# Performance work log

Measured on AMD Instinct MI355X. Metric: run time of the kernel, lower is better.

## Reference

```python
import jax, jax.numpy as jnp
import numpy as np

EPS = 1e-6
NEG_SLOPE = 0.2


def knn_idx(xf, k):
    # xf: (B, C, N) flattened vector features; returns (B, N, k) neighbor indices
    xx = jnp.sum(xf * xf, axis=1)                       # (B, N)
    inner = jnp.einsum('bcn,bcm->bnm', xf, xf)          # (B, N, N)
    neg_dist = 2.0 * inner - xx[:, :, None] - xx[:, None, :]  # -||xi-xj||^2
    _, idx = jax.lax.top_k(neg_dist, k)                 # includes self (dist 0)
    return idx


def get_graph_feature(x, k):
    # x: (B, D, 3, N) -> edge features (B, 2D, 3, N, k)
    B, D, _, N = x.shape
    idx = knn_idx(x.reshape(B, D * 3, N), k)            # (B, N, k)
    pts = jnp.transpose(x, (0, 3, 1, 2))                # (B, N, D, 3)
    neigh = jax.vmap(lambda p, i: p[i])(pts, idx)       # (B, N, k, D, 3) gather
    center = jnp.broadcast_to(pts[:, :, None], neigh.shape)
    feat = jnp.concatenate([neigh - center, center], axis=3)  # (B, N, k, 2D, 3)
    return jnp.transpose(feat, (0, 3, 4, 1, 2))


def vn_linear_leakyrelu(x, Wf, Wd):
    # Vector-Neuron linear + leaky ReLU. x: (B, Cin, 3, ...),
    # Wf: (Cout, Cin), Wd: (Cout, Cin) or (1, Cin) when nonlinearity is shared.
    p = jnp.einsum('oi,bi...->bo...', Wf, x)
    d = jnp.einsum('oi,bi...->bo...', Wd, x)
    dot = jnp.sum(p * d, axis=2, keepdims=True)
    dsq = jnp.sum(d * d, axis=2, keepdims=True)
    proj = p - (dot / (dsq + EPS)) * d
    return NEG_SLOPE * p + (1.0 - NEG_SLOPE) * jnp.where(dot >= 0, p, proj)


def setup_inputs() -> dict:
    key = jax.random.key(0)
    ks = jax.random.split(key, 11)
    B, N = 8, 1024
    x = jax.random.normal(ks[0], (B, 3, N), dtype=jnp.float32)
    # dims = [1, 21, 21, 42, 85, 341]
    ins = [2, 42, 42, 84, 169]      # 2*dim_in for edge layers; sum(dims[1:-1]) for last
    outs = [21, 21, 42, 85, 341]
    dirs = [21, 21, 42, 85, 1]      # last layer has share_nonlinearity=True
    d = {"x": x}
    for i, (ci, co, cd) in enumerate(zip(ins, outs, dirs)):
        s = 1.0 / np.sqrt(ci)
        kf, kd = jax.random.split(ks[1 + i])
        d[f"Wf{i}"] = (jax.random.normal(kf, (co, ci), dtype=jnp.float32) * s)
        d[f"Wd{i}"] = (jax.random.normal(kd, (cd, ci), dtype=jnp.float32) * s)
    d["k"] = 20
    return d


def reference(x, Wf0, Wd0, Wf1, Wd1, Wf2, Wd2, Wf3, Wd3, Wf4, Wd4, k):
    cur = x[:, None]                 # (B, 1, 3, N)
    feats = []
    for Wf, Wd in ((Wf0, Wd0), (Wf1, Wd1), (Wf2, Wd2), (Wf3, Wd3)):
        g = get_graph_feature(cur, k)        # (B, 2D, 3, N, k)
        h = vn_linear_leakyrelu(g, Wf, Wd)   # (B, Dout, 3, N, k)
        cur = h.mean(axis=-1)                # mean over neighbors -> (B, Dout, 3, N)
        feats.append(cur)
    xcat = jnp.concatenate(feats, axis=1)    # (B, 169, 3, N)
    out = vn_linear_leakyrelu(xcat, Wf4, Wd4)
    return out.mean(axis=-1)                 # mean over points -> (B, 341, 3)
```

## Files before the change

kernel.cpp:

```cpp
#include <hip/hip_runtime.h>
#include <cstddef>

#define BB 8
#define NN 1024
#define KK 20
#define CCAT 169
#define NT 16

__global__ __launch_bounds__(256) void dist_tile_kernel(
    const float* __restrict__ src, int bs, int F, float* __restrict__ dist) {
  __shared__ float As[8][128];
  __shared__ float Bs[8][128];
  int b = blockIdx.z;
  int rem = blockIdx.x, bi = 0;
  while (rem >= 8 - bi) { rem -= 8 - bi; ++bi; }
  int bj = bi + rem;
  int n0 = bi * 128;
  int m0 = bj * 128;
  int t = threadIdx.x;
  int tx = t & 15, ty = t >> 4;
  const float* p = src + (size_t)b * bs;

  float acc[8][8];
  float xn[8], xm[8];
#pragma unroll
  for (int i = 0; i < 8; ++i) {
    xn[i] = 0.f;
    xm[i] = 0.f;
#pragma unroll
    for (int j = 0; j < 8; ++j) acc[i][j] = 0.f;
  }

  int fr = t >> 5;
  int cc = (t & 31) << 2;
  for (int f0 = 0; f0 < F; f0 += 8) {
    int f = f0 + fr;
    float4 av = {0.f, 0.f, 0.f, 0.f}, bv = {0.f, 0.f, 0.f, 0.f};
    if (f < F) {
      av = *(const float4*)(p + (size_t)f * NN + n0 + cc);
      bv = *(const float4*)(p + (size_t)f * NN + m0 + cc);
    }
    __syncthreads();
    *(float4*)&As[fr][cc] = av;
    *(float4*)&Bs[fr][cc] = bv;
    __syncthreads();
#pragma unroll
    for (int f2 = 0; f2 < 8; ++f2) {
      float4 al = *(const float4*)&As[f2][ty << 2];
      float4 ah = *(const float4*)&As[f2][64 + (ty << 2)];
      float4 bl = *(const float4*)&Bs[f2][tx << 2];
      float4 bh = *(const float4*)&Bs[f2][64 + (tx << 2)];
      float a[8] = {al.x, al.y, al.z, al.w, ah.x, ah.y, ah.z, ah.w};
      float bb[8] = {bl.x, bl.y, bl.z, bl.w, bh.x, bh.y, bh.z, bh.w};
#pragma unroll
      for (int i = 0; i < 8; ++i) xn[i] += a[i] * a[i];
#pragma unroll
      for (int j = 0; j < 8; ++j) xm[j] += bb[j] * bb[j];
#pragma unroll
      for (int i = 0; i < 8; ++i)
#pragma unroll
        for (int j = 0; j < 8; ++j) acc[i][j] += a[i] * bb[j];
    }
  }

#pragma unroll
  for (int i = 0; i < 8; ++i)
#pragma unroll
    for (int j = 0; j < 8; ++j) acc[i][j] = 2.f * acc[i][j] - xn[i] - xm[j];

#pragma unroll
  for (int i = 0; i < 8; ++i) {
    int n = n0 + ((i < 4) ? ((ty << 2) + i) : (64 + (ty << 2) + i - 4));
    float* dr = dist + (((size_t)b * NN + n) << 10);
    *(float4*)(dr + m0 + (tx << 2)) =
        make_float4(acc[i][0], acc[i][1], acc[i][2], acc[i][3]);
    *(float4*)(dr + m0 + 64 + (tx << 2)) =
        make_float4(acc[i][4], acc[i][5], acc[i][6], acc[i][7]);
  }

  if (bi != bj) {
#pragma unroll
    for (int j = 0; j < 8; ++j) {
      int m = m0 + ((j < 4) ? ((tx << 2) + j) : (64 + (tx << 2) + j - 4));
      float* dr = dist + (((size_t)b * NN + m) << 10);
      *(float4*)(dr + n0 + (ty << 2)) =
          make_float4(acc[0][j], acc[1][j], acc[2][j], acc[3][j]);
      *(float4*)(dr + n0 + 64 + (ty << 2)) =
          make_float4(acc[4][j], acc[5][j], acc[6][j], acc[7][j]);
    }
  }
}

__device__ __forceinline__ unsigned long long shfl_xor_u64(
    unsigned long long v, int off) {
  unsigned lo = (unsigned)v, hi = (unsigned)(v >> 32);
  lo = __shfl_xor(lo, off, 64);
  hi = __shfl_xor(hi, off, 64);
  return ((unsigned long long)hi << 32) | lo;
}

__global__ __launch_bounds__(256) void topk_kernel(
    const float* __restrict__ dist, int* __restrict__ idx_out) {
  int wave = threadIdx.x >> 6;
  int lane = threadIdx.x & 63;
  int row = blockIdx.x * 4 + wave;
  const float* d = dist + ((size_t)row << 10);

  unsigned long long key[16];
#pragma unroll
  for (int s = 0; s < 16; ++s) {
    int m = lane + (s << 6);
    unsigned u = __float_as_uint(d[m]);
    u = (u & 0x80000000u) ? ~u : (u | 0x80000000u);
    key[s] = ((unsigned long long)u << 32) | (unsigned)(NN - 1 - m);
  }

#pragma unroll
  for (int size = 2; size <= 16; size <<= 1) {
#pragma unroll
    for (int stride = size >> 1; stride > 0; stride >>= 1) {
#pragma unroll
      for (int i = 0; i < 16; ++i) {
        int j = i ^ stride;
        if (j > i) {
          unsigned long long a = key[i], c = key[j];
          bool desc = ((i & size) == 0);
          bool sw = desc ? (a < c) : (a > c);
          key[i] = sw ? c : a;
          key[j] = sw ? a : c;
        }
      }
    }
  }

  int* out = idx_out + row * KK;
  unsigned long long head = key[0];
  for (int r = 0; r < KK; ++r) {
    unsigned long long w = head;
#pragma unroll
    for (int off = 32; off > 0; off >>= 1) {
      unsigned long long o = shfl_xor_u64(w, off);
      if (o > w) w = o;
    }
    if (lane == 0) out[r] = (NN - 1) - (int)(w & 0xFFFFFFFFull);
    if (head == w) {
#pragma unroll
      for (int s = 0; s < 15; ++s) key[s] = key[s + 1];
      key[15] = 0ull;
      head = key[0];
    }
  }
}

__global__ __launch_bounds__(256) void edge_fused_kernel(
    const float* __restrict__ src, int bs, int D, int Co, int nsplit,
    const float* __restrict__ Wf, const float* __restrict__ Wd,
    const int* __restrict__ idx, int ooff, float* __restrict__ xcat) {
  __shared__ float2 Ulds[3 * NN];
  __shared__ float2 Vlds[3 * NN];
  __shared__ float4 Wlds[48];
  int bo = blockIdx.x;
  int b = bo / Co, o = bo % Co;
  int t = threadIdx.x;

  if (t < D) {
    float wfa = Wf[o * 2 * D + t];
    float wfb = Wf[o * 2 * D + D + t] - wfa;
    float wda = Wd[o * 2 * D + t];
    float wdb = Wd[o * 2 * D + D + t] - wda;
    Wlds[t] = make_float4(wfa, wfb, wda, wdb);
  }
  __syncthreads();

  const float* sb = src + (size_t)b * bs;
#pragma unroll
  for (int r = 0; r < 3; ++r) {
    int g = t + 256 * r;
    float4 uf = {0.f, 0.f, 0.f, 0.f}, vf = {0.f, 0.f, 0.f, 0.f};
    float4 ud = {0.f, 0.f, 0.f, 0.f}, vd = {0.f, 0.f, 0.f, 0.f};
    for (int i = 0; i < D; ++i) {
      float4 s = *(const float4*)(sb + (size_t)i * 3 * NN + (g << 2));
      float4 w = Wlds[i];
      uf.x += w.x * s.x; uf.y += w.x * s.y; uf.z += w.x * s.z; uf.w += w.x * s.w;
      vf.x += w.y * s.x; vf.y += w.y * s.y; vf.z += w.y * s.z; vf.w += w.y * s.w;
      ud.x += w.z * s.x; ud.y += w.z * s.y; ud.z += w.z * s.z; ud.w += w.z * s.w;
      vd.x += w.w * s.x; vd.y += w.w * s.y; vd.z += w.w * s.z; vd.w += w.w * s.w;
    }
    *(float4*)&Ulds[(g << 2) + 0] = make_float4(uf.x, ud.x, uf.y, ud.y);
    *(float4*)&Ulds[(g << 2) + 2] = make_float4(uf.z, ud.z, uf.w, ud.w);
    *(float4*)&Vlds[(g << 2) + 0] = make_float4(vf.x, vd.x, vf.y, vd.y);
    *(float4*)&Vlds[(g << 2) + 2] = make_float4(vf.z, vd.z, vf.w, vd.w);
  }
  __syncthreads();

  const float inv_k = 1.f / KK;
  int cnt = NN / nsplit;
  int nbase = blockIdx.y * cnt;
  for (int n = nbase + t; n < nbase + cnt; n += 256) {
    float2 v0 = Vlds[n];
    float2 v1 = Vlds[NN + n];
    float2 v2 = Vlds[2 * NN + n];
    const int4* ip = (const int4*)(idx + (b * NN + n) * KK);
    float a0 = 0.f, a1 = 0.f, a2 = 0.f;
#pragma unroll
    for (int q = 0; q < 5; ++q) {
      int4 iv = ip[q];
      int nbs[4] = {iv.x, iv.y, iv.z, iv.w};
#pragma unroll
      for (int jj = 0; jj < 4; ++jj) {
        int nb = nbs[jj];
        float2 u0 = Ulds[nb];
        float2 u1 = Ulds[NN + nb];
        float2 u2 = Ulds[2 * NN + nb];
        float pf0 = u0.x + v0.x, pd0 = u0.y + v0.y;
        float pf1 = u1.x + v1.x, pd1 = u1.y + v1.y;
        float pf2 = u2.x + v2.x, pd2 = u2.y + v2.y;
        float dot = pf0 * pd0 + pf1 * pd1 + pf2 * pd2;
        float dsq = pd0 * pd0 + pd1 * pd1 + pd2 * pd2;
        float g = (dot >= 0.f) ? 0.f : 0.8f * dot / (dsq + 1e-6f);
        a0 += pf0 - g * pd0;
        a1 += pf1 - g * pd1;
        a2 += pf2 - g * pd2;
      }
    }
    size_t ob = (size_t)b * CCAT * 3 * NN + (size_t)(ooff + o) * 3 * NN + n;
    xcat[ob] = a0 * inv_k;
    xcat[ob + NN] = a1 * inv_k;
    xcat[ob + 2 * NN] = a2 * inv_k;
  }
}

__global__ __launch_bounds__(256) void final_fused_kernel(
    const float* __restrict__ xcat, const float* __restrict__ Wf4,
    const float* __restrict__ Wd4, float* __restrict__ part) {
  __shared__ float Ws[16][64];
  __shared__ float Xs[3][16][64];
  __shared__ float Wds[16];
  int b = blockIdx.z;
  int o0 = blockIdx.y * 64;
  int n0 = blockIdx.x * 64;
  int t = threadIdx.x;
  int tx = t & 15, ty = t >> 4;

  float acc[3][4][4];
  float dv[3][4];
#pragma unroll
  for (int c = 0; c < 3; ++c) {
#pragma unroll
    for (int i = 0; i < 4; ++i)
#pragma unroll
      for (int j = 0; j < 4; ++j) acc[c][i][j] = 0.f;
#pragma unroll
    for (int j = 0; j < 4; ++j) dv[c][j] = 0.f;
  }

  const float* xb = xcat + (size_t)b * CCAT * 3 * NN;
  for (int f0 = 0; f0 < CCAT; f0 += 16) {
    int f = f0 + ty;
    float4 xv[3];
#pragma unroll
    for (int c = 0; c < 3; ++c) {
      xv[c] = make_float4(0.f, 0.f, 0.f, 0.f);
      if (f < CCAT)
        xv[c] = *(const float4*)(xb + ((size_t)f * 3 + c) * NN + n0 + (tx << 2));
    }
    float wv[4];
#pragma unroll
    for (int q = 0; q < 4; ++q) {
      int o = o0 + (tx << 2) + q;
      wv[q] = (o < 341 && f < CCAT) ? Wf4[o * CCAT + f] : 0.f;
    }
    float wdv = 0.f;
    if (t < 16 && f0 + t < CCAT) wdv = Wd4[f0 + t];
    __syncthreads();
#pragma unroll
    for (int c = 0; c < 3; ++c) *(float4*)&Xs[c][ty][tx << 2] = xv[c];
    *(float4*)&Ws[ty][tx << 2] = make_float4(wv[0], wv[1], wv[2], wv[3]);
    if (t < 16) Wds[t] = wdv;
    __syncthreads();
#pragma unroll
    for (int f2 = 0; f2 < 16; ++f2) {
      float4 w = *(const float4*)&Ws[f2][ty << 2];
      float wa[4] = {w.x, w.y, w.z, w.w};
      float wd = Wds[f2];
#pragma unroll
      for (int c = 0; c < 3; ++c) {
        float4 x = *(const float4*)&Xs[c][f2][tx << 2];
        float xa[4] = {x.x, x.y, x.z, x.w};
#pragma unroll
        for (int j = 0; j < 4; ++j) dv[c][j] += wd * xa[j];
#pragma unroll
        for (int i = 0; i < 4; ++i)
#pragma unroll
          for (int j = 0; j < 4; ++j) acc[c][i][j] += wa[i] * xa[j];
      }
    }
  }

  float s[3][4];
#pragma unroll
  for (int c = 0; c < 3; ++c)
#pragma unroll
    for (int i = 0; i < 4; ++i) s[c][i] = 0.f;
#pragma unroll
  for (int i = 0; i < 4; ++i) {
#pragma unroll
    for (int j = 0; j < 4; ++j) {
      float d0 = dv[0][j], d1 = dv[1][j], d2 = dv[2][j];
      float p0 = acc[0][i][j], p1 = acc[1][i][j], p2 = acc[2][i][j];
      float dot = p0 * d0 + p1 * d1 + p2 * d2;
      float dsq = d0 * d0 + d1 * d1 + d2 * d2;
      float g = (dot >= 0.f) ? 0.f : 0.8f * dot / (dsq + 1e-6f);
      s[0][i] += p0 - g * d0;
      s[1][i] += p1 - g * d1;
      s[2][i] += p2 - g * d2;
    }
  }

#pragma unroll
  for (int off = 1; off < 16; off <<= 1) {
#pragma unroll
    for (int c = 0; c < 3; ++c)
#pragma unroll
      for (int i = 0; i < 4; ++i) s[c][i] += __shfl_xor(s[c][i], off, 64);
  }
  if (tx == 0) {
#pragma unroll
    for (int i = 0; i < 4; ++i) {
      int o = o0 + (ty << 2) + i;
      if (o < 341) {
#pragma unroll
        for (int c = 0; c < 3; ++c)
          part[(((size_t)b * 341 + o) * 3 + c) * NT + blockIdx.x] = s[c][i];
      }
    }
  }
}

__global__ void final_reduce_kernel(const float* __restrict__ part,
                                    float* __restrict__ out) {
  int t = blockIdx.x * 256 + threadIdx.x;
  if (t >= BB * 341 * 3) return;
  const float* p = part + (size_t)t * NT;
  float s = 0.f;
#pragma unroll
  for (int nt = 0; nt < NT; ++nt) s += p[nt];
  out[t] = s * (1.f / 1024.f);
}

extern "C" void kernel_launch(void* const* d_in, const int* in_sizes, int n_in,
                              void* d_out, int out_size, void* d_ws,
                              size_t ws_size, hipStream_t stream) {
  (void)in_sizes; (void)n_in; (void)out_size; (void)ws_size;
  const float* x = (const float*)d_in[0];
  const float* Wf[5] = {(const float*)d_in[1], (const float*)d_in[3],
                        (const float*)d_in[5], (const float*)d_in[7],
                        (const float*)d_in[9]};
  const float* Wd[5] = {(const float*)d_in[2], (const float*)d_in[4],
                        (const float*)d_in[6], (const float*)d_in[8],
                        (const float*)d_in[10]};

  float* ws = (float*)d_ws;
  float* dist = ws;
  float* part = ws;
  size_t off = (size_t)BB * NN * NN;
  int* idx = (int*)(ws + off);
  off += (size_t)BB * NN * KK;
  float* xcat = ws + off;

  struct LayerCfg { int D, Co, inoff, ooff, nsplit; };
  const LayerCfg L[4] = {
      {1, 21, 0, 0, 4},
      {21, 21, 0, 21, 4},
      {21, 42, 21, 42, 2},
      {42, 85, 42, 84, 1},
  };

  for (int l = 0; l < 4; ++l) {
    const float* src = (l == 0) ? x : (xcat + (size_t)L[l].inoff * 3 * NN);
    int bs = (l == 0) ? 3 * NN : CCAT * 3 * NN;
    int D = L[l].D, Co = L[l].Co;

    dist_tile_kernel<<<dim3(36, 1, BB), 256, 0, stream>>>(src, bs, 3 * D, dist);
    topk_kernel<<<(BB * NN) / 4, 256, 0, stream>>>(dist, idx);
    edge_fused_kernel<<<dim3(BB * Co, L[l].nsplit), 256, 0, stream>>>(
        src, bs, D, Co, L[l].nsplit, Wf[l], Wd[l], idx, L[l].ooff, xcat);
  }

  final_fused_kernel<<<dim3(NT, 6, BB), 256, 0, stream>>>(xcat, Wf[4], Wd[4],
                                                          part);
  final_reduce_kernel<<<(BB * 341 * 3 + 255) / 256, 256, 0, stream>>>(
      part, (float*)d_out);
}
```

Before: 431.8 us.

## Split edge kernel into tiled transform GEMM and gather, retile final kernel

The per-output-channel edge kernel, which recomputed the U/V linear transform over the whole point set with a naive per-thread loop, is split into a shared-memory tiled transform kernel that writes U/V to workspace and a gather kernel that loads them into LDS and does the neighbor aggregation. This reuses source feature tiles across 16 output channels instead of re-reading the inputs once per channel. It costs an extra launch and a global round trip for U/V, which reuse the distance-matrix workspace. Separately, the final kernel's output tile is halved to 32 channels to launch more blocks, and the last layer's gather now uses two splits.

```diff
diff --git a/kernel.cpp b/kernel.cpp
--- a/kernel.cpp
+++ b/kernel.cpp
@@ -152,46 +152,98 @@
   }
 }
 
-__global__ __launch_bounds__(256) void edge_fused_kernel(
-    const float* __restrict__ src, int bs, int D, int Co, int nsplit,
+__global__ __launch_bounds__(256) void transform_kernel(
+    const float* __restrict__ src, int bs, int D, int Co,
     const float* __restrict__ Wf, const float* __restrict__ Wd,
-    const int* __restrict__ idx, int ooff, float* __restrict__ xcat) {
-  __shared__ float2 Ulds[3 * NN];
-  __shared__ float2 Vlds[3 * NN];
-  __shared__ float4 Wlds[48];
+    float2* __restrict__ ubuf, float2* __restrict__ vbuf) {
+  __shared__ float4 Slds4[16][32];
+  __shared__ float4 Wlds[16][16];
+  int b = blockIdx.z;
+  int g0 = blockIdx.x * 128;
+  int o0 = blockIdx.y * 16;
+  int t = threadIdx.x;
+  int tx = t & 15, ty = t >> 4;
+  const float* sb = src + (size_t)b * bs;
+
+  float uf[8], ud[8], vf[8], vd[8];
+#pragma unroll
+  for (int g = 0; g < 8; ++g) { uf[g] = 0.f; ud[g] = 0.f; vf[g] = 0.f; vd[g] = 0.f; }
+
+  for (int f0 = 0; f0 < D; f0 += 16) {
+    float4 w4 = {0.f, 0.f, 0.f, 0.f};
+    {
+      int i = f0 + tx;
+      int o = o0 + ty;
+      if (i < D && o < Co) {
+        float wfa = Wf[o * 2 * D + i];
+        float wfb = Wf[o * 2 * D + D + i];
+        float wda = Wd[o * 2 * D + i];
+        float wdb = Wd[o * 2 * D + D + i];
+        w4 = make_float4(wfa, wfb - wfa, wda, wdb - wda);
+      }
+    }
+    int q0 = t, q1 = t + 256;
+    int r0 = q0 >> 5, c0 = q0 & 31;
+    int r1 = q1 >> 5, c1 = q1 & 31;
+    float4 s0 = {0.f, 0.f, 0.f, 0.f}, s1 = {0.f, 0.f, 0.f, 0.f};
+    if (f0 + r0 < D)
+      s0 = *(const float4*)(sb + (size_t)(f0 + r0) * 3 * NN + g0 + (c0 << 2));
+    if (f0 + r1 < D)
+      s1 = *(const float4*)(sb + (size_t)(f0 + r1) * 3 * NN + g0 + (c1 << 2));
+    __syncthreads();
+    Wlds[tx][ty] = w4;
+    Slds4[r0][c0] = s0;
+    Slds4[r1][c1] = s1;
+    __syncthreads();
+#pragma unroll
+    for (int k = 0; k < 16; ++k) {
+      float4 w = Wlds[k][ty];
+      float4 sA = Slds4[k][tx << 1];
+      float4 sB = Slds4[k][(tx << 1) + 1];
+      float sg[8] = {sA.x, sA.y, sA.z, sA.w, sB.x, sB.y, sB.z, sB.w};
+#pragma unroll
+      for (int g = 0; g < 8; ++g) {
+        uf[g] += w.x * sg[g];
+        vf[g] += w.y * sg[g];
+        ud[g] += w.z * sg[g];
+        vd[g] += w.w * sg[g];
+      }
+    }
+    __syncthreads();
+  }
+
+  int o = o0 + ty;
+  if (o < Co) {
+    size_t base = ((size_t)b * Co + o) * 3072 + g0 + (tx << 3);
+    float4* up = (float4*)(ubuf + base);
+    float4* vp = (float4*)(vbuf + base);
+#pragma unroll
+    for (int g2 = 0; g2 < 4; ++g2) {
+      up[g2] = make_float4(uf[2 * g2], ud[2 * g2], uf[2 * g2 + 1], ud[2 * g2 + 1]);
+      vp[g2] = make_float4(vf[2 * g2], vd[2 * g2], vf[2 * g2 + 1], vd[2 * g2 + 1]);
+    }
+  }
+}
+
+__global__ __launch_bounds__(256) void gather_kernel(
+    const float2* __restrict__ ubuf, const float2* __restrict__ vbuf, int Co,
+    int nsplit, const int* __restrict__ idx, int ooff,
+    float* __restrict__ xcat) {
+  __shared__ float4 U4[1536];
+  __shared__ float4 V4[1536];
   int bo = blockIdx.x;
   int b = bo / Co, o = bo % Co;
   int t = threadIdx.x;
-
-  if (t < D) {
-    float wfa = Wf[o * 2 * D + t];
-    float wfb = Wf[o * 2 * D + D + t] - wfa;
-    float wda = Wd[o * 2 * D + t];
-    float wdb = Wd[o * 2 * D + D + t] - wda;
-    Wlds[t] = make_float4(wfa, wfb, wda, wdb);
+  const float4* usrc = (const float4*)(ubuf + ((size_t)b * Co + o) * 3072);
+  const float4* vsrc = (const float4*)(vbuf + ((size_t)b * Co + o) * 3072);
+#pragma unroll
+  for (int r = 0; r < 6; ++r) {
+    U4[t + 256 * r] = usrc[t + 256 * r];
+    V4[t + 256 * r] = vsrc[t + 256 * r];
   }
   __syncthreads();
-
-  const float* sb = src + (size_t)b * bs;
-#pragma unroll
-  for (int r = 0; r < 3; ++r) {
-    int g = t + 256 * r;
-    float4 uf = {0.f, 0.f, 0.f, 0.f}, vf = {0.f, 0.f, 0.f, 0.f};
-    float4 ud = {0.f, 0.f, 0.f, 0.f}, vd = {0.f, 0.f, 0.f, 0.f};
-    for (int i = 0; i < D; ++i) {
-      float4 s = *(const float4*)(sb + (size_t)i * 3 * NN + (g << 2));
-      float4 w = Wlds[i];
-      uf.x += w.x * s.x; uf.y += w.x * s.y; uf.z += w.x * s.z; uf.w += w.x * s.w;
-      vf.x += w.y * s.x; vf.y += w.y * s.y; vf.z += w.y * s.z; vf.w += w.y * s.w;
-      ud.x += w.z * s.x; ud.y += w.z * s.y; ud.z += w.z * s.z; ud.w += w.z * s.w;
-      vd.x += w.w * s.x; vd.y += w.w * s.y; vd.z += w.w * s.z; vd.w += w.w * s.w;
-    }
-    *(float4*)&Ulds[(g << 2) + 0] = make_float4(uf.x, ud.x, uf.y, ud.y);
-    *(float4*)&Ulds[(g << 2) + 2] = make_float4(uf.z, ud.z, uf.w, ud.w);
-    *(float4*)&Vlds[(g << 2) + 0] = make_float4(vf.x, vd.x, vf.y, vd.y);
-    *(float4*)&Vlds[(g << 2) + 2] = make_float4(vf.z, vd.z, vf.w, vd.w);
-  }
-  __syncthreads();
+  const float2* Ulds = (const float2*)U4;
+  const float2* Vlds = (const float2*)V4;
 
   const float inv_k = 1.f / KK;
   int cnt = NN / nsplit;
@@ -233,21 +285,21 @@
 __global__ __launch_bounds__(256) void final_fused_kernel(
     const float* __restrict__ xcat, const float* __restrict__ Wf4,
     const float* __restrict__ Wd4, float* __restrict__ part) {
-  __shared__ float Ws[16][64];
+  __shared__ float Ws[16][32];
   __shared__ float Xs[3][16][64];
   __shared__ float Wds[16];
   int b = blockIdx.z;
-  int o0 = blockIdx.y * 64;
+  int o0 = blockIdx.y * 32;
   int n0 = blockIdx.x * 64;
   int t = threadIdx.x;
   int tx = t & 15, ty = t >> 4;
 
-  float acc[3][4][4];
+  float acc[3][2][4];
   float dv[3][4];
 #pragma unroll
   for (int c = 0; c < 3; ++c) {
 #pragma unroll
-    for (int i = 0; i < 4; ++i)
+    for (int i = 0; i < 2; ++i)
 #pragma unroll
       for (int j = 0; j < 4; ++j) acc[c][i][j] = 0.f;
 #pragma unroll
@@ -264,24 +316,26 @@
       if (f < CCAT)
         xv[c] = *(const float4*)(xb + ((size_t)f * 3 + c) * NN + n0 + (tx << 2));
     }
-    float wv[4];
-#pragma unroll
-    for (int q = 0; q < 4; ++q) {
-      int o = o0 + (tx << 2) + q;
-      wv[q] = (o < 341 && f < CCAT) ? Wf4[o * CCAT + f] : 0.f;
+    float wv0 = 0.f, wv1 = 0.f;
+    {
+      int oa = o0 + tx, ob = o0 + tx + 16;
+      if (f < CCAT) {
+        if (oa < 341) wv0 = Wf4[oa * CCAT + f];
+        if (ob < 341) wv1 = Wf4[ob * CCAT + f];
+      }
     }
     float wdv = 0.f;
     if (t < 16 && f0 + t < CCAT) wdv = Wd4[f0 + t];
     __syncthreads();
 #pragma unroll
     for (int c = 0; c < 3; ++c) *(float4*)&Xs[c][ty][tx << 2] = xv[c];
-    *(float4*)&Ws[ty][tx << 2] = make_float4(wv[0], wv[1], wv[2], wv[3]);
+    Ws[ty][tx] = wv0;
+    Ws[ty][tx + 16] = wv1;
     if (t < 16) Wds[t] = wdv;
     __syncthreads();
 #pragma unroll
     for (int f2 = 0; f2 < 16; ++f2) {
-      float4 w = *(const float4*)&Ws[f2][ty << 2];
-      float wa[4] = {w.x, w.y, w.z, w.w};
+      float2 w = *(const float2*)&Ws[f2][ty << 1];
       float wd = Wds[f2];
 #pragma unroll
       for (int c = 0; c < 3; ++c) {
@@ -290,20 +344,21 @@
 #pragma unroll
         for (int j = 0; j < 4; ++j) dv[c][j] += wd * xa[j];
 #pragma unroll
-        for (int i = 0; i < 4; ++i)
-#pragma unroll
-          for (int j = 0; j < 4; ++j) acc[c][i][j] += wa[i] * xa[j];
-      }
-    }
-  }
-
-  float s[3][4];
+        for (int j = 0; j < 4; ++j) {
+          acc[c][0][j] += w.x * xa[j];
+          acc[c][1][j] += w.y * xa[j];
+        }
+      }
+    }
+  }
+
+  float s[3][2];
 #pragma unroll
   for (int c = 0; c < 3; ++c)
 #pragma unroll
-    for (int i = 0; i < 4; ++i) s[c][i] = 0.f;
-#pragma unroll
-  for (int i = 0; i < 4; ++i) {
+    for (int i = 0; i < 2; ++i) s[c][i] = 0.f;
+#pragma unroll
+  for (int i = 0; i < 2; ++i) {
 #pragma unroll
     for (int j = 0; j < 4; ++j) {
       float d0 = dv[0][j], d1 = dv[1][j], d2 = dv[2][j];
@@ -322,12 +377,12 @@
 #pragma unroll
     for (int c = 0; c < 3; ++c)
 #pragma unroll
-      for (int i = 0; i < 4; ++i) s[c][i] += __shfl_xor(s[c][i], off, 64);
+      for (int i = 0; i < 2; ++i) s[c][i] += __shfl_xor(s[c][i], off, 64);
   }
   if (tx == 0) {
 #pragma unroll
-    for (int i = 0; i < 4; ++i) {
-      int o = o0 + (ty << 2) + i;
+    for (int i = 0; i < 2; ++i) {
+      int o = o0 + (ty << 1) + i;
       if (o < 341) {
 #pragma unroll
         for (int c = 0; c < 3; ++c)
@@ -363,6 +418,8 @@
   float* ws = (float*)d_ws;
   float* dist = ws;
   float* part = ws;
+  float2* ubuf = (float2*)ws;
+  float2* vbuf = (float2*)(ws + (size_t)BB * 85 * 3072 * 2);
   size_t off = (size_t)BB * NN * NN;
   int* idx = (int*)(ws + off);
   off += (size_t)BB * NN * KK;
@@ -373,7 +430,7 @@
       {1, 21, 0, 0, 4},
       {21, 21, 0, 21, 4},
       {21, 42, 21, 42, 2},
-      {42, 85, 42, 84, 1},
+      {42, 85, 42, 84, 2},
   };
 
   for (int l = 0; l < 4; ++l) {
@@ -383,12 +440,14 @@
 
     dist_tile_kernel<<<dim3(36, 1, BB), 256, 0, stream>>>(src, bs, 3 * D, dist);
     topk_kernel<<<(BB * NN) / 4, 256, 0, stream>>>(dist, idx);
-    edge_fused_kernel<<<dim3(BB * Co, L[l].nsplit), 256, 0, stream>>>(
-        src, bs, D, Co, L[l].nsplit, Wf[l], Wd[l], idx, L[l].ooff, xcat);
-  }
-
-  final_fused_kernel<<<dim3(NT, 6, BB), 256, 0, stream>>>(xcat, Wf[4], Wd[4],
-                                                          part);
+    transform_kernel<<<dim3(24, (Co + 15) / 16, BB), 256, 0, stream>>>(
+        src, bs, D, Co, Wf[l], Wd[l], ubuf, vbuf);
+    gather_kernel<<<dim3(BB * Co, L[l].nsplit), 256, 0, stream>>>(
+        ubuf, vbuf, Co, L[l].nsplit, idx, L[l].ooff, xcat);
+  }
+
+  final_fused_kernel<<<dim3(NT, 11, BB), 256, 0, stream>>>(xcat, Wf[4], Wd[4],
+                                                           part);
   final_reduce_kernel<<<(BB * 341 * 3 + 255) / 256, 256, 0, stream>>>(
       part, (float*)d_out);
 }
```

After: 490.9 us. 1.14x slower.
